# Kernel tuning notes

Measured on AMD Instinct MI355X. Metric: run time of the kernel, lower is better.

## Reference

```python
import jax, jax.numpy as jnp
import numpy as np

S, D, H, C, A = 2048, 256, 8, 64, 16  # seq_len, node_dim, num_heads, num_channels, num_aux


def setup_inputs() -> dict:
    key = jax.random.key(0)
    ks = jax.random.split(key, 11)
    w = 0.02
    return {
        "nodes": jax.random.normal(ks[0], (S, D), jnp.float32),
        "pos": jax.random.uniform(ks[1], (S, 3), jnp.float32),
        "aux": jax.random.normal(ks[2], (S, A), jnp.float32),
        # eqx.nn.Linear weights are (out_features, in_features); y = W @ x + b
        "W_nodes_kq": jax.random.normal(ks[3], (2 * H * C, D), jnp.float32) * w,
        "b_nodes_kq": jax.random.normal(ks[4], (2 * H * C,), jnp.float32) * w,
        "W_pos_kq": jax.random.normal(ks[5], (2 * H * C, 6), jnp.float32) * w,
        "b_pos_kq": jax.random.normal(ks[6], (2 * H * C,), jnp.float32) * w,
        "W_aux_kq": jax.random.normal(ks[7], (2 * H * C, A), jnp.float32) * w,  # no bias
        "W_val": jax.random.normal(ks[8], (D * H * 3, D), jnp.float32) * w,
        "b_val": jax.random.normal(ks[9], (D * H * 3,), jnp.float32) * w,
        "num_heads": H,
    }


def reference(nodes, pos, aux, W_nodes_kq, b_nodes_kq, W_pos_kq, b_pos_kq,
              W_aux_kq, W_val, b_val, num_heads):
    seq_len = nodes.shape[0]
    # circular positional featurization: [S, 6]
    pos_f = jnp.concatenate([jnp.cos(2 * jnp.pi * pos), jnp.sin(2 * jnp.pi * pos)], axis=-1)
    # values: [S, 3*H, D]
    val = (nodes @ W_val.T + b_val).reshape(seq_len, 3 * num_heads, -1)
    # k/q projections, each reshaped [S, H, 2C] then split into k, q of [S, H, C]
    nodes_k, nodes_q = jnp.split((nodes @ W_nodes_kq.T + b_nodes_kq).reshape(seq_len, num_heads, -1), 2, -1)
    pos_k, pos_q = jnp.split((pos_f @ W_pos_kq.T + b_pos_kq).reshape(seq_len, num_heads, -1), 2, -1)
    aux_k, aux_q = jnp.split((aux @ W_aux_kq.T).reshape(seq_len, num_heads, -1), 2, -1)
    # concat along the HEAD axis -> [S, 3H, C]
    k = jnp.concatenate([nodes_k, pos_k, aux_k], axis=-2)
    q = jnp.concatenate([nodes_q, pos_q, aux_q], axis=-2)
    # all-pairs logits [S, S, 3H]; softmax over the SECOND (query, j) index
    logits = jnp.einsum('ihc,jhc->ijh', k, q)
    att = jax.nn.softmax(logits, axis=-2)
    # weighted sum over j and heads -> [S, D]
    out = jnp.einsum('ijh,jhd->id', att, val)
    return out
```

## Files before the change

kernel.cpp:

```cpp
#include <hip/hip_runtime.h>
#include <math.h>

#define SLEN 2048
#define ND 256
#define NH 24
#define HC 64
#define TWO_PI 6.283185307179586f
#define NT 64

typedef __attribute__((ext_vector_type(8))) short short8;
typedef __attribute__((ext_vector_type(16))) float f32x16;
typedef __attribute__((ext_vector_type(2))) unsigned int uint2e;

static __device__ __forceinline__ unsigned short f2bf(float f) {
    union { float f; unsigned int u; } v; v.f = f;
    unsigned int u = v.u;
    return (unsigned short)((u + 0x7FFFu + ((u >> 16) & 1u)) >> 16);
}
static __device__ __forceinline__ unsigned int pack2(float a, float b) {
    return (unsigned int)f2bf(a) | ((unsigned int)f2bf(b) << 16);
}
static __device__ __forceinline__ unsigned int cvtpk(float lo, float hi) {
    unsigned int r;
    asm("v_cvt_pk_bf16_f32 %0, %1, %2" : "=v"(r) : "v"(lo), "v"(hi));
    return r;
}
static __device__ __forceinline__ void gload_lds16(const void* g, void* l) {
    __builtin_amdgcn_global_load_lds(
        (const __attribute__((address_space(1))) void*)(g),
        (__attribute__((address_space(3))) void*)(l), 16, 0, 0);
}

__global__ __launch_bounds__(256) void zero_partial_kernel(float4* __restrict__ p) {
    p[(size_t)blockIdx.x * 256 + threadIdx.x] = make_float4(0.f, 0.f, 0.f, 0.f);
}

__global__ __launch_bounds__(256) void f32_to_bf16_kernel(
    const float4* __restrict__ in, uint2* __restrict__ out) {
    const size_t id = (size_t)blockIdx.x * 256 + threadIdx.x;
    float4 v = in[id];
    uint2 u; u.x = pack2(v.x, v.y); u.y = pack2(v.z, v.w);
    out[id] = u;
}

__global__ __launch_bounds__(256) void posf_kernel(
    const float* __restrict__ pos, float* __restrict__ pos_f) {
    const int s = blockIdx.x * 256 + threadIdx.x;
    if (s < SLEN) {
        #pragma unroll
        for (int c = 0; c < 3; ++c) {
            float v = pos[s * 3 + c] * TWO_PI;
            pos_f[s * 8 + c] = cosf(v);
            pos_f[s * 8 + 3 + c] = sinf(v);
        }
        pos_f[s * 8 + 6] = 0.f; pos_f[s * 8 + 7] = 0.f;
    }
}

__global__ __launch_bounds__(256) void gemm_kernel(
    const unsigned short* __restrict__ wv_bf, const unsigned short* __restrict__ wn_bf,
    const unsigned short* __restrict__ nodes_bf, const float* __restrict__ bv,
    unsigned short* __restrict__ vt, float* __restrict__ kqtmp)
{
    __shared__ __align__(16) char lds[131072];
    const int tid = threadIdx.x;
    const int w = tid >> 6, lane = tid & 63;
    const int l31 = lane & 31, lh = lane >> 5;
    const int bid = blockIdx.x;
    const bool isval = bid < 768;
    int o0, s0;
    const unsigned short *Aptr, *Bptr;
    if (isval) {
        const int wg = ((bid & 7) * 96) + (bid >> 3);
        o0 = (wg >> 4) * 128; s0 = (wg & 15) * 128;
        Aptr = wv_bf + (size_t)o0 * 256; Bptr = nodes_bf + (size_t)s0 * 256;
    } else {
        const int b = bid - 768;
        o0 = (b >> 4) * 128; s0 = (b & 15) * 128;
        Aptr = nodes_bf + (size_t)s0 * 256; Bptr = wn_bf + (size_t)o0 * 256;
    }

    {
        const int rbase = w * 32;
        const int roff = lane >> 5;
        const int slot = l31 * 16;
        #pragma unroll
        for (int i = 0; i < 16; ++i) {
            const int row = rbase + i * 2 + roff;
            const int colb = slot ^ ((row & 31) << 4);
            gload_lds16(Aptr + (((size_t)row) << 8) + (colb >> 1),
                        lds + (rbase + i * 2) * 512);
        }
        #pragma unroll
        for (int i = 0; i < 16; ++i) {
            const int row = rbase + i * 2 + roff;
            const int colb = slot ^ ((row & 31) << 4);
            gload_lds16(Bptr + (((size_t)row) << 8) + (colb >> 1),
                        lds + 65536 + (rbase + i * 2) * 512);
        }
    }
    __syncthreads();

    const int wm = w >> 1, wn = w & 1;
    f32x16 acc[2][2];
    #pragma unroll
    for (int mf = 0; mf < 2; ++mf)
        #pragma unroll
        for (int nf = 0; nf < 2; ++nf)
            #pragma unroll
            for (int r = 0; r < 16; ++r) acc[mf][nf][r] = 0.f;

    const char* Abase = lds;
    const char* Bbase = lds + 65536;
    #pragma unroll
    for (int kk = 0; kk < 16; ++kk) {
        short8 af[2], bq[2];
        #pragma unroll
        for (int mf = 0; mf < 2; ++mf) {
            const int row = wm * 64 + mf * 32 + l31;
            af[mf] = *(const short8*)(Abase + row * 512 +
                     ((kk * 32 + lh * 16) ^ ((row & 31) << 4)));
        }
        #pragma unroll
        for (int nf = 0; nf < 2; ++nf) {
            const int row = wn * 64 + nf * 32 + l31;
            bq[nf] = *(const short8*)(Bbase + row * 512 +
                     ((kk * 32 + lh * 16) ^ ((row & 31) << 4)));
        }
        #pragma unroll
        for (int mf = 0; mf < 2; ++mf)
            #pragma unroll
            for (int nf = 0; nf < 2; ++nf)
                acc[mf][nf] = __builtin_amdgcn_mfma_f32_32x32x16_bf16(
                    af[mf], bq[nf], acc[mf][nf], 0, 0, 0);
    }

    if (isval) {
        #pragma unroll
        for (int mf = 0; mf < 2; ++mf) {
            #pragma unroll
            for (int r = 0; r < 16; ++r) {
                const int o = o0 + wm * 64 + mf * 32 + (r & 3) + 8 * (r >> 2) + 4 * lh;
                const float b = bv[o];
                #pragma unroll
                for (int nf = 0; nf < 2; ++nf) {
                    const int s = s0 + wn * 64 + nf * 32 + l31;
                    vt[(size_t)o * SLEN + s] = f2bf(acc[mf][nf][r] + b);
                }
            }
        }
    } else {
        #pragma unroll
        for (int mf = 0; mf < 2; ++mf) {
            #pragma unroll
            for (int r = 0; r < 16; ++r) {
                const int srow = s0 + wm * 64 + mf * 32 + (r & 3) + 8 * (r >> 2) + 4 * lh;
                #pragma unroll
                for (int nf = 0; nf < 2; ++nf) {
                    const int o = o0 + wn * 64 + nf * 32 + l31;
                    kqtmp[(size_t)srow * 1024 + o] = acc[mf][nf][r];
                }
            }
        }
    }
}

__global__ __launch_bounds__(256) void kq_epi_kernel(
    const float* __restrict__ kqtmp, const float* __restrict__ pos_f,
    const float* __restrict__ aux, const float* __restrict__ bn,
    const float* __restrict__ bp, const float* __restrict__ Wp,
    const float* __restrict__ Wa,
    unsigned short* __restrict__ kbf, unsigned short* __restrict__ qbf)
{
    const int tid = threadIdx.x;
    const int s = blockIdx.x >> 2;
    const int o = (blockIdx.x & 3) * 256 + tid;

    const float vn = kqtmp[(size_t)s * 1024 + o] + bn[o];
    float vp = bp[o];
    #pragma unroll
    for (int d = 0; d < 6; ++d) vp += pos_f[s * 8 + d] * Wp[o * 6 + d];
    float va = 0.f;
    #pragma unroll
    for (int d = 0; d < 16; ++d) va += aux[s * 16 + d] * Wa[o * 16 + d];

    const int h8 = o >> 7, rem = o & 127, isq = rem >> 6, c = rem & 63;
    unsigned short* dst = isq ? qbf : kbf;
    dst[((size_t)h8 * SLEN + s) * HC + c]        = f2bf(vn);
    dst[((size_t)(8 + h8) * SLEN + s) * HC + c]  = f2bf(vp);
    dst[((size_t)(16 + h8) * SLEN + s) * HC + c] = f2bf(va);
}

__global__ __launch_bounds__(256, 3) void attn_kernel(
    const unsigned short* __restrict__ kbf, const unsigned short* __restrict__ qbf,
    const unsigned short* __restrict__ vt, float* __restrict__ partial)
{
    __shared__ __align__(16) char smem[40960];

    const int tid = threadIdx.x;
    const int w = tid >> 6, lane = tid & 63;
    const int l31 = lane & 31, lh = lane >> 5;
    const int wi = w >> 1, wd = w & 1;
    const int wg = (blockIdx.x & 7) * 96 + (blockIdx.x >> 3);
    const int h = wg >> 5, it = wg & 31;
    const int i0 = it * 64;

    const unsigned short* kh = kbf + (size_t)h * SLEN * HC;
    const unsigned short* qh = qbf + (size_t)h * SLEN * HC;
    const unsigned short* vh = vt + (size_t)h * ND * SLEN;

    short8 kf[4];
    {
        const unsigned short* kp = kh + (size_t)(i0 + wi * 32 + l31) * HC + lh * 8;
        #pragma unroll
        for (int ks = 0; ks < 4; ++ks) kf[ks] = *(const short8*)(kp + ks * 16);
    }

    f32x16 acc[4];
    #pragma unroll
    for (int nf = 0; nf < 4; ++nf)
        #pragma unroll
        for (int r = 0; r < 16; ++r) acc[nf][r] = 0.f;
    float m_run = -1e30f, l_run = 0.f;

    auto stage = [&](int bufo, int jt) {
        const int j0n = jt * 32;
        #pragma unroll
        for (int i = 0; i < 5; ++i) {
            const int c = i * 4 + w;
            const int lrow = (lane >> 3);
            const int cu = (((lane & 7) << 4) ^ (lrow << 4));
            if (c < 4) {
                const int row = c * 8 + lrow;
                gload_lds16(qh + (size_t)(j0n + row) * HC + (cu >> 1),
                            smem + bufo + c * 1024);
            } else {
                const int row = (c - 4) * 8 + lrow;
                const int d = row * 2 + (cu >> 6);
                const int j = (cu & 63) >> 1;
                gload_lds16(vh + (size_t)d * SLEN + j0n + j,
                            smem + bufo + 4096 + (c - 4) * 1024);
            }
        }
    };

    auto softpack = [&](f32x16& S, uint4& p0, uint4& p1) {
        float tmax = S[0];
        #pragma unroll
        for (int r = 1; r < 16; ++r) tmax = fmaxf(tmax, S[r]);
        tmax = fmaxf(tmax, __shfl_xor(tmax, 32));
        if (!__all(tmax - m_run <= 8.0f)) {
            const float mnew = fmaxf(m_run, tmax);
            const float sc = __expf(m_run - mnew);
            l_run *= sc; m_run = mnew;
            #pragma unroll
            for (int r = 0; r < 16; ++r) {
                const float scv = __shfl(sc, (r & 3) + 8 * (r >> 2) + 4 * lh);
                #pragma unroll
                for (int nf = 0; nf < 4; ++nf) acc[nf][r] *= scv;
            }
        }
        float psum = 0.f;
        #pragma unroll
        for (int r = 0; r < 16; ++r) {
            S[r] = __expf(S[r] - m_run);
            psum += S[r];
        }
        psum += __shfl_xor(psum, 32);
        l_run += psum;
        uint2e r1 = __builtin_amdgcn_permlane32_swap(cvtpk(S[0], S[1]), cvtpk(S[4], S[5]), false, false);
        uint2e r2 = __builtin_amdgcn_permlane32_swap(cvtpk(S[2], S[3]), cvtpk(S[6], S[7]), false, false);
        uint2e r3 = __builtin_amdgcn_permlane32_swap(cvtpk(S[8], S[9]), cvtpk(S[12], S[13]), false, false);
        uint2e r4 = __builtin_amdgcn_permlane32_swap(cvtpk(S[10], S[11]), cvtpk(S[14], S[15]), false, false);
        p0 = make_uint4(r1[0], r2[0], r1[1], r2[1]);
        p1 = make_uint4(r3[0], r4[0], r3[1], r4[1]);
    };

    stage(0, 0);
    __syncthreads();

    for (int jt = 0; jt < NT; ++jt) {
        const int bo = (jt & 1) * 20480;
        if (jt + 1 < NT) stage(20480 - bo, jt + 1);
        const char* qb = smem + bo;
        const char* vb = smem + bo + 4096;

        f32x16 S;
        #pragma unroll
        for (int r = 0; r < 16; ++r) S[r] = 0.f;
        const int qsw = (l31 & 7) << 4;
        __builtin_amdgcn_s_setprio(1);
        #pragma unroll
        for (int ks = 0; ks < 4; ++ks) {
            short8 a = *(const short8*)(qb + l31 * 128 + ((ks * 32 + lh * 16) ^ qsw));
            S = __builtin_amdgcn_mfma_f32_32x32x16_bf16(a, kf[ks], S, 0, 0, 0);
        }
        __builtin_amdgcn_s_setprio(0);

        uint4 p0, p1;
        softpack(S, p0, p1);

        __builtin_amdgcn_s_setprio(1);
        #pragma unroll
        for (int ksl = 0; ksl < 2; ++ksl) {
            const short8 pa = *(const short8*)(ksl ? &p1 : &p0);
            #pragma unroll
            for (int nf = 0; nf < 4; ++nf) {
                const int d = wd * 128 + nf * 32 + l31;
                const int row = d >> 1;
                const int colb = (((d & 1) << 6) + ksl * 32 + lh * 16) ^ ((row & 7) << 4);
                short8 vfrag = *(const short8*)(vb + row * 128 + colb);
                acc[nf] = __builtin_amdgcn_mfma_f32_32x32x16_bf16(pa, vfrag, acc[nf], 0, 0, 0);
            }
        }
        __builtin_amdgcn_s_setprio(0);
        __syncthreads();
    }

    float* pb = partial + (size_t)(h / 3) * (SLEN * ND);
    const float invm = 1.0f / l_run;
    float lv[16];
    #pragma unroll
    for (int r = 0; r < 16; ++r)
        lv[r] = __shfl(invm, (r & 3) + 8 * (r >> 2) + 4 * lh);
    #pragma unroll
    for (int nf = 0; nf < 4; ++nf) {
        const int d = wd * 128 + nf * 32 + l31;
        #pragma unroll
        for (int r = 0; r < 16; ++r) {
            const int i = i0 + wi * 32 + (r & 3) + 8 * (r >> 2) + 4 * lh;
            atomicAdd(pb + (size_t)i * ND + d, acc[nf][r] * lv[r]);
        }
    }
}

__global__ __launch_bounds__(256) void reduce_kernel(
    const float4* __restrict__ partial, float4* __restrict__ out)
{
    const size_t id = (size_t)blockIdx.x * 256 + threadIdx.x;
    float4 s = make_float4(0.f, 0.f, 0.f, 0.f);
    #pragma unroll
    for (int g = 0; g < 8; ++g) {
        float4 v = partial[g * (SLEN * ND / 4) + id];
        s.x += v.x; s.y += v.y; s.z += v.z; s.w += v.w;
    }
    out[id] = s;
}

extern "C" void kernel_launch(void* const* d_in, const int* in_sizes, int n_in,
                              void* d_out, int out_size, void* d_ws, size_t ws_size,
                              hipStream_t stream) {
    const float* nodes = (const float*)d_in[0];
    const float* pos   = (const float*)d_in[1];
    const float* aux   = (const float*)d_in[2];
    const float* Wn    = (const float*)d_in[3];
    const float* bn    = (const float*)d_in[4];
    const float* Wp    = (const float*)d_in[5];
    const float* bp    = (const float*)d_in[6];
    const float* Wa    = (const float*)d_in[7];
    const float* Wv    = (const float*)d_in[8];
    const float* bv    = (const float*)d_in[9];
    float* out = (float*)d_out;

    const size_t KQ   = (size_t)SLEN * NH * HC;
    const size_t VT   = (size_t)NH * ND * SLEN;
    const size_t WVBF = (size_t)6144 * ND;
    const size_t WNBF = (size_t)1024 * ND;
    const size_t NDBF = (size_t)SLEN * ND;
    const size_t POSF = (size_t)SLEN * 8;
    const size_t KQT  = (size_t)SLEN * 1024;
    const size_t PART = (size_t)8 * SLEN * ND;
    const size_t need = (2 * KQ + VT + WVBF + WNBF + NDBF) * 2 + (POSF + KQT + PART) * 4;

    if (ws_size < need) return;

    unsigned short* kbf = (unsigned short*)d_ws;
    unsigned short* qbf = kbf + KQ;
    unsigned short* vt  = qbf + KQ;
    unsigned short* wv_bf = vt + VT;
    unsigned short* wn_bf = wv_bf + WVBF;
    unsigned short* nodes_bf = wn_bf + WNBF;
    float* pos_f   = (float*)(nodes_bf + NDBF);
    float* kqtmp   = pos_f + POSF;
    float* partial = kqtmp + KQT;

    zero_partial_kernel<<<PART / 1024, 256, 0, stream>>>((float4*)partial);
    f32_to_bf16_kernel<<<1536, 256, 0, stream>>>((const float4*)Wv, (uint2*)wv_bf);
    f32_to_bf16_kernel<<<256, 256, 0, stream>>>((const float4*)Wn, (uint2*)wn_bf);
    f32_to_bf16_kernel<<<512, 256, 0, stream>>>((const float4*)nodes, (uint2*)nodes_bf);
    posf_kernel<<<8, 256, 0, stream>>>(pos, pos_f);
    gemm_kernel<<<896, 256, 0, stream>>>(wv_bf, wn_bf, nodes_bf, bv, vt, kqtmp);
    kq_epi_kernel<<<8192, 256, 0, stream>>>(kqtmp, pos_f, aux, bn, bp, Wp, Wa, kbf, qbf);
    attn_kernel<<<768, 256, 0, stream>>>(kbf, qbf, vt, partial);
    reduce_kernel<<<512, 256, 0, stream>>>((const float4*)partial, (float4*)out);
}
```

Before: 173.5 us.

## Fuse k/q epilogue into GEMM and split softmax from PV across attention waves

```diff
diff --git a/kernel.cpp b/kernel.cpp
--- a/kernel.cpp
+++ b/kernel.cpp
@@ -6,6 +6,7 @@
 #define NH 24
 #define HC 64
 #define TWO_PI 6.283185307179586f
+#define LOG2E 1.4426950408889634f
 #define NT 64
 
 typedef __attribute__((ext_vector_type(8))) short short8;
@@ -29,10 +30,6 @@
     __builtin_amdgcn_global_load_lds(
         (const __attribute__((address_space(1))) void*)(g),
         (__attribute__((address_space(3))) void*)(l), 16, 0, 0);
-}
-
-__global__ __launch_bounds__(256) void zero_partial_kernel(float4* __restrict__ p) {
-    p[(size_t)blockIdx.x * 256 + threadIdx.x] = make_float4(0.f, 0.f, 0.f, 0.f);
 }
 
 __global__ __launch_bounds__(256) void f32_to_bf16_kernel(
@@ -60,7 +57,11 @@
 __global__ __launch_bounds__(256) void gemm_kernel(
     const unsigned short* __restrict__ wv_bf, const unsigned short* __restrict__ wn_bf,
     const unsigned short* __restrict__ nodes_bf, const float* __restrict__ bv,
-    unsigned short* __restrict__ vt, float* __restrict__ kqtmp)
+    unsigned short* __restrict__ vt,
+    const float* __restrict__ pos_f, const float* __restrict__ aux,
+    const float* __restrict__ bn, const float* __restrict__ bp,
+    const float* __restrict__ Wp, const float* __restrict__ Wa,
+    unsigned short* __restrict__ kbf, unsigned short* __restrict__ qbf)
 {
     __shared__ __align__(16) char lds[131072];
     const int tid = threadIdx.x;
@@ -150,52 +151,57 @@
             }
         }
     } else {
-        #pragma unroll
-        for (int mf = 0; mf < 2; ++mf) {
-            #pragma unroll
-            for (int r = 0; r < 16; ++r) {
-                const int srow = s0 + wm * 64 + mf * 32 + (r & 3) + 8 * (r >> 2) + 4 * lh;
+        __syncthreads();
+        float* pa_lds = (float*)lds;
+        for (int i = tid; i < 128 * 6; i += 256) {
+            const int srow = i / 6, q4 = i % 6;
+            float4 v;
+            if (q4 < 2) v = *(const float4*)(pos_f + (size_t)(s0 + srow) * 8 + q4 * 4);
+            else        v = *(const float4*)(aux + (size_t)(s0 + srow) * 16 + (q4 - 2) * 4);
+            *(float4*)(pa_lds + srow * 24 + q4 * 4) = v;
+        }
+        __syncthreads();
+        #pragma unroll
+        for (int nf = 0; nf < 2; ++nf) {
+            const int o = o0 + wn * 64 + nf * 32 + l31;
+            float wp[6], wa[16];
+            #pragma unroll
+            for (int d = 0; d < 6; ++d) wp[d] = Wp[(size_t)o * 6 + d];
+            #pragma unroll
+            for (int d = 0; d < 16; ++d) wa[d] = Wa[(size_t)o * 16 + d];
+            const float bno = bn[o], bpo = bp[o];
+            const int h8 = o >> 7, rem = o & 127, isq = rem >> 6, c = rem & 63;
+            unsigned short* dst = isq ? qbf : kbf;
+            const float ksc = isq ? 1.0f : LOG2E;
+            #pragma unroll
+            for (int mf = 0; mf < 2; ++mf) {
                 #pragma unroll
-                for (int nf = 0; nf < 2; ++nf) {
-                    const int o = o0 + wn * 64 + nf * 32 + l31;
-                    kqtmp[(size_t)srow * 1024 + o] = acc[mf][nf][r];
+                for (int r = 0; r < 16; ++r) {
+                    const int sl = wm * 64 + mf * 32 + (r & 3) + 8 * (r >> 2) + 4 * lh;
+                    const int s = s0 + sl;
+                    const float* pr = pa_lds + sl * 24;
+                    const float vn = acc[mf][nf][r] + bno;
+                    float vp = bpo;
+                    #pragma unroll
+                    for (int d = 0; d < 6; ++d) vp += pr[d] * wp[d];
+                    float va = 0.f;
+                    #pragma unroll
+                    for (int d = 0; d < 16; ++d) va += pr[8 + d] * wa[d];
+                    dst[((size_t)h8 * SLEN + s) * HC + c]        = f2bf(vn * ksc);
+                    dst[((size_t)(8 + h8) * SLEN + s) * HC + c]  = f2bf(vp * ksc);
+                    dst[((size_t)(16 + h8) * SLEN + s) * HC + c] = f2bf(va * ksc);
                 }
             }
         }
     }
-}
-
-__global__ __launch_bounds__(256) void kq_epi_kernel(
-    const float* __restrict__ kqtmp, const float* __restrict__ pos_f,
-    const float* __restrict__ aux, const float* __restrict__ bn,
-    const float* __restrict__ bp, const float* __restrict__ Wp,
-    const float* __restrict__ Wa,
-    unsigned short* __restrict__ kbf, unsigned short* __restrict__ qbf)
-{
-    const int tid = threadIdx.x;
-    const int s = blockIdx.x >> 2;
-    const int o = (blockIdx.x & 3) * 256 + tid;
-
-    const float vn = kqtmp[(size_t)s * 1024 + o] + bn[o];
-    float vp = bp[o];
-    #pragma unroll
-    for (int d = 0; d < 6; ++d) vp += pos_f[s * 8 + d] * Wp[o * 6 + d];
-    float va = 0.f;
-    #pragma unroll
-    for (int d = 0; d < 16; ++d) va += aux[s * 16 + d] * Wa[o * 16 + d];
-
-    const int h8 = o >> 7, rem = o & 127, isq = rem >> 6, c = rem & 63;
-    unsigned short* dst = isq ? qbf : kbf;
-    dst[((size_t)h8 * SLEN + s) * HC + c]        = f2bf(vn);
-    dst[((size_t)(8 + h8) * SLEN + s) * HC + c]  = f2bf(vp);
-    dst[((size_t)(16 + h8) * SLEN + s) * HC + c] = f2bf(va);
 }
 
 __global__ __launch_bounds__(256, 3) void attn_kernel(
     const unsigned short* __restrict__ kbf, const unsigned short* __restrict__ qbf,
     const unsigned short* __restrict__ vt, float* __restrict__ partial)
 {
-    __shared__ __align__(16) char smem[40960];
+    __shared__ __align__(16) char smem[45312];
+    const int BUF = 20480, VOFF = 4096, POFF = 40960, SCOFF = 45056;
 
     const int tid = threadIdx.x;
     const int w = tid >> 6, lane = tid & 63;
@@ -223,82 +229,114 @@
         for (int r = 0; r < 16; ++r) acc[nf][r] = 0.f;
     float m_run = -1e30f, l_run = 0.f;
 
+    auto stage_chunk = [&](int bufo, int j0n, int c) {
+        if (c < 4) {
+            const int row = c * 8 + (lane >> 3);
+            const int cb = ((lane & 7) << 4) ^ ((row & 7) << 4);
+            gload_lds16(qh + (size_t)(j0n + row) * HC + (cb >> 1),
+                        smem + bufo + c * 1024);
+        } else {
+            const int cc = c - 4;
+            const int d = cc * 16 + (lane >> 2);
+            const int jb = ((lane & 3) << 4) ^ (((d >> 1) & 3) << 4);
+            gload_lds16(vh + (size_t)d * SLEN + j0n + (jb >> 1),
+                        smem + bufo + VOFF + cc * 1024);
+        }
+    };
     auto stage = [&](int bufo, int jt) {
         const int j0n = jt * 32;
-        #pragma unroll
-        for (int i = 0; i < 5; ++i) {
-            const int c = i * 4 + w;
-            const int lrow = (lane >> 3);
-            const int cu = (((lane & 7) << 4) ^ (lrow << 4));
-            if (c < 4) {
-                const int row = c * 8 + lrow;
-                gload_lds16(qh + (size_t)(j0n + row) * HC + (cu >> 1),
-                            smem + bufo + c * 1024);
-            } else {
-                const int row = (c - 4) * 8 + lrow;
-                const int d = row * 2 + (cu >> 6);
-                const int j = (cu & 63) >> 1;
-                gload_lds16(vh + (size_t)d * SLEN + j0n + j,
-                            smem + bufo + 4096 + (c - 4) * 1024);
-            }
-        }
-    };
-
-    auto softpack = [&](f32x16& S, uint4& p0, uint4& p1) {
-        float tmax = S[0];
-        #pragma unroll
-        for (int r = 1; r < 16; ++r) tmax = fmaxf(tmax, S[r]);
-        tmax = fmaxf(tmax, __shfl_xor(tmax, 32));
-        if (!__all(tmax - m_run <= 8.0f)) {
-            const float mnew = fmaxf(m_run, tmax);
-            const float sc = __expf(m_run - mnew);
-            l_run *= sc; m_run = mnew;
-            #pragma unroll
-            for (int r = 0; r < 16; ++r) {
-                const float scv = __shfl(sc, (r & 3) + 8 * (r >> 2) + 4 * lh);
-                #pragma unroll
-                for (int nf = 0; nf < 4; ++nf) acc[nf][r] *= scv;
-            }
-        }
-        float psum = 0.f;
-        #pragma unroll
-        for (int r = 0; r < 16; ++r) {
-            S[r] = __expf(S[r] - m_run);
-            psum += S[r];
-        }
-        psum += __shfl_xor(psum, 32);
-        l_run += psum;
-        uint2e r1 = __builtin_amdgcn_permlane32_swap(cvtpk(S[0], S[1]), cvtpk(S[4], S[5]), false, false);
-        uint2e r2 = __builtin_amdgcn_permlane32_swap(cvtpk(S[2], S[3]), cvtpk(S[6], S[7]), false, false);
-        uint2e r3 = __builtin_amdgcn_permlane32_swap(cvtpk(S[8], S[9]), cvtpk(S[12], S[13]), false, false);
-        uint2e r4 = __builtin_amdgcn_permlane32_swap(cvtpk(S[10], S[11]), cvtpk(S[14], S[15]), false, false);
-        p0 = make_uint4(r1[0], r2[0], r1[1], r2[1]);
-        p1 = make_uint4(r3[0], r4[0], r3[1], r4[1]);
+        if (wd == 0) {
+            const int st = (w == 0) ? 0 : 10;
+            #pragma unroll
+            for (int i = 0; i < 3; ++i) stage_chunk(bufo, j0n, st + i);
+        } else {
+            const int st = (w == 1) ? 3 : 13;
+            #pragma unroll
+            for (int i = 0; i < 7; ++i) stage_chunk(bufo, j0n, st + i);
+        }
     };
 
     stage(0, 0);
     __syncthreads();
 
     for (int jt = 0; jt < NT; ++jt) {
-        const int bo = (jt & 1) * 20480;
-        if (jt + 1 < NT) stage(20480 - bo, jt + 1);
+        const int bo = (jt & 1) * BUF;
+        if (jt + 1 < NT) stage(BUF - bo, jt + 1);
         const char* qb = smem + bo;
-        const char* vb = smem + bo + 4096;
-
-        f32x16 S;
-        #pragma unroll
-        for (int r = 0; r < 16; ++r) S[r] = 0.f;
-        const int qsw = (l31 & 7) << 4;
-        __builtin_amdgcn_s_setprio(1);
-        #pragma unroll
-        for (int ks = 0; ks < 4; ++ks) {
-            short8 a = *(const short8*)(qb + l31 * 128 + ((ks * 32 + lh * 16) ^ qsw));
-            S = __builtin_amdgcn_mfma_f32_32x32x16_bf16(a, kf[ks], S, 0, 0, 0);
-        }
-        __builtin_amdgcn_s_setprio(0);
+        const char* vb = smem + bo + VOFF;
 
         uint4 p0, p1;
-        softpack(S, p0, p1);
+        if (wd == 0) {
+            f32x16 S;
+            #pragma unroll
+            for (int r = 0; r < 16; ++r) S[r] = 0.f;
+            const int qsw = (l31 & 7) << 4;
+            __builtin_amdgcn_s_setprio(1);
+            #pragma unroll
+            for (int ks = 0; ks < 4; ++ks) {
+                short8 a = *(const short8*)(qb + l31 * 128 + ((ks * 32 + lh * 16) ^ qsw));
+                S = __builtin_amdgcn_mfma_f32_32x32x16_bf16(a, kf[ks], S, 0, 0, 0);
+            }
+            __builtin_amdgcn_s_setprio(0);
+
+            float t0 = fmaxf(fmaxf(S[0], S[1]), S[2]);
+            float t1 = fmaxf(fmaxf(S[3], S[4]), S[5]);
+            float t2 = fmaxf(fmaxf(S[6], S[7]), S[8]);
+            float t3 = fmaxf(fmaxf(S[9], S[10]), S[11]);
+            float t4 = fmaxf(fmaxf(S[12], S[13]), S[14]);
+            float tmax = fmaxf(fmaxf(fmaxf(t0, t1), fmaxf(t2, t3)), fmaxf(t4, S[15]));
+            tmax = fmaxf(tmax, __shfl_xor(tmax, 32));
+
+            float scw = 1.0f;
+            if (!__all(tmax - m_run <= 8.0f)) {
+                const float mnew = fmaxf(m_run, tmax);
+                scw = exp2f(m_run - mnew);
+                l_run *= scw; m_run = mnew;
+                #pragma unroll
+                for (int r = 0; r < 16; ++r) {
+                    const float scv = __shfl(scw, (r & 3) + 8 * (r >> 2) + 4 * lh);
+                    #pragma unroll
+                    for (int nf = 0; nf < 4; ++nf) acc[nf][r] *= scv;
+                }
+            }
+            if (lane < 32) *(float*)(smem + SCOFF + wi * 128 + l31 * 4) = scw;
+
+            float psum = 0.f;
+            #pragma unroll
+            for (int r = 0; r < 16; ++r) {
+                S[r] = exp2f(S[r] - m_run);
+                psum += S[r];
+            }
+            psum += __shfl_xor(psum, 32);
+            l_run += psum;
+
+            uint2e r1 = __builtin_amdgcn_permlane32_swap(cvtpk(S[0], S[1]), cvtpk(S[4], S[5]), false, false);
+            uint2e r2 = __builtin_amdgcn_permlane32_swap(cvtpk(S[2], S[3]), cvtpk(S[6], S[7]), false, false);
+            uint2e r3 = __builtin_amdgcn_permlane32_swap(cvtpk(S[8], S[9]), cvtpk(S[12], S[13]), false, false);
+            uint2e r4 = __builtin_amdgcn_permlane32_swap(cvtpk(S[10], S[11]), cvtpk(S[14], S[15]), false, false);
+            p0 = make_uint4(r1[0], r2[0], r1[1], r2[1]);
+            p1 = make_uint4(r3[0], r4[0], r3[1], r4[1]);
+            *(uint4*)(smem + POFF + wi * 2048 + lane * 16) = p0;
+            *(uint4*)(smem + POFF + wi * 2048 + 1024 + lane * 16) = p1;
+        }
+
+        asm volatile("s_waitcnt lgkmcnt(0)" ::: "memory");
+        __builtin_amdgcn_s_barrier();
+        asm volatile("" ::: "memory");
+
+        if (wd == 1) {
+            p0 = *(const uint4*)(smem + POFF + wi * 2048 + lane * 16);
+            p1 = *(const uint4*)(smem + POFF + wi * 2048 + 1024 + lane * 16);
+            const float scr = *(const float*)(smem + SCOFF + wi * 128 + l31 * 4);
+            if (!__all(scr == 1.0f)) {
+                #pragma unroll
+                for (int r = 0; r < 16; ++r) {
+                    const float scv = __shfl(scr, (r & 3) + 8 * (r >> 2) + 4 * lh);
+                    #pragma unroll
+                    for (int nf = 0; nf < 4; ++nf) acc[nf][r] *= scv;
+                }
+            }
+        }
 
         __builtin_amdgcn_s_setprio(1);
         #pragma unroll
@@ -307,9 +345,8 @@
             #pragma unroll
             for (int nf = 0; nf < 4; ++nf) {
                 const int d = wd * 128 + nf * 32 + l31;
-                const int row = d >> 1;
-                const int colb = (((d & 1) << 6) + ksl * 32 + lh * 16) ^ ((row & 7) << 4);
-                short8 vfrag = *(const short8*)(vb + row * 128 + colb);
+                const int slot = (ksl * 32 + lh * 16) ^ (((d >> 1) & 3) << 4);
+                short8 vfrag = *(const short8*)(vb + d * 64 + slot);
                 acc[nf] = __builtin_amdgcn_mfma_f32_32x32x16_bf16(pa, vfrag, acc[nf], 0, 0, 0);
             }
         }
@@ -317,12 +354,15 @@
         __syncthreads();
     }
 
+    if (wd == 0 && lane < 32)
+        *(float*)(smem + SCOFF + wi * 128 + l31 * 4) = 1.0f / l_run;
+    __syncthreads();
+    const float invl = *(const float*)(smem + SCOFF + wi * 128 + l31 * 4);
+    float lv[16];
+    #pragma unroll
+    for (int r = 0; r < 16; ++r)
+        lv[r] = __shfl(invl, (r & 3) + 8 * (r >> 2) + 4 * lh);
     float* pb = partial + (size_t)(h / 3) * (SLEN * ND);
-    const float invm = 1.0f / l_run;
-    float lv[16];
-    #pragma unroll
-    for (int r = 0; r < 16; ++r)
-        lv[r] = __shfl(invm, (r & 3) + 8 * (r >> 2) + 4 * lh);
     #pragma unroll
     for (int nf = 0; nf < 4; ++nf) {
         const int d = wd * 128 + nf * 32 + l31;
@@ -368,9 +408,8 @@
     const size_t WNBF = (size_t)1024 * ND;
     const size_t NDBF = (size_t)SLEN * ND;
     const size_t POSF = (size_t)SLEN * 8;
-    const size_t KQT  = (size_t)SLEN * 1024;
     const size_t PART = (size_t)8 * SLEN * ND;
-    const size_t need = (2 * KQ + VT + WVBF + WNBF + NDBF) * 2 + (POSF + KQT + PART) * 4;
+    const size_t need = (2 * KQ + VT + WVBF + WNBF + NDBF) * 2 + (POSF + PART) * 4;
 
     if (ws_size < need) return;
 
@@ -381,16 +420,15 @@
     unsigned short* wn_bf = wv_bf + WVBF;
     unsigned short* nodes_bf = wn_bf + WNBF;
     float* pos_f   = (float*)(nodes_bf + NDBF);
-    float* kqtmp   = pos_f + POSF;
-    float* partial = kqtmp + KQT;
-
-    zero_partial_kernel<<<PART / 1024, 256, 0, stream>>>((float4*)partial);
+    float* partial = pos_f + POSF;
+
+    hipMemsetAsync(partial, 0, PART * sizeof(float), stream);
     f32_to_bf16_kernel<<<1536, 256, 0, stream>>>((const float4*)Wv, (uint2*)wv_bf);
     f32_to_bf16_kernel<<<256, 256, 0, stream>>>((const float4*)Wn, (uint2*)wn_bf);
     f32_to_bf16_kernel<<<512, 256, 0, stream>>>((const float4*)nodes, (uint2*)nodes_bf);
     posf_kernel<<<8, 256, 0, stream>>>(pos, pos_f);
-    gemm_kernel<<<896, 256, 0, stream>>>(wv_bf, wn_bf, nodes_bf, bv, vt, kqtmp);
-    kq_epi_kernel<<<8192, 256, 0, stream>>>(kqtmp, pos_f, aux, bn, bp, Wp, Wa, kbf, qbf);
+    gemm_kernel<<<896, 256, 0, stream>>>(wv_bf, wn_bf, nodes_bf, bv, vt,
+                                         pos_f, aux, bn, bp, Wp, Wa, kbf, qbf);
     attn_kernel<<<768, 256, 0, stream>>>(kbf, qbf, vt, partial);
     reduce_kernel<<<512, 256, 0, stream>>>((const float4*)partial, (float4*)out);
 }
```

New measurement: 305.1 us. 1.76x slower.

## Fuse node k/q bias epilogue into GEMM and switch softmax to exp2

Applied to the files above, without the earlier changes.

```diff
diff --git a/kernel.cpp b/kernel.cpp
--- a/kernel.cpp
+++ b/kernel.cpp
@@ -6,6 +6,7 @@
 #define NH 24
 #define HC 64
 #define TWO_PI 6.283185307179586f
+#define LOG2E 1.4426950408889634f
 #define NT 64
 
 typedef __attribute__((ext_vector_type(8))) short short8;
@@ -25,14 +26,13 @@
     asm("v_cvt_pk_bf16_f32 %0, %1, %2" : "=v"(r) : "v"(lo), "v"(hi));
     return r;
 }
+static __device__ __forceinline__ float exp2fast(float x) {
+    return __builtin_amdgcn_exp2f(x);
+}
 static __device__ __forceinline__ void gload_lds16(const void* g, void* l) {
     __builtin_amdgcn_global_load_lds(
         (const __attribute__((address_space(1))) void*)(g),
         (__attribute__((address_space(3))) void*)(l), 16, 0, 0);
-}
-
-__global__ __launch_bounds__(256) void zero_partial_kernel(float4* __restrict__ p) {
-    p[(size_t)blockIdx.x * 256 + threadIdx.x] = make_float4(0.f, 0.f, 0.f, 0.f);
 }
 
 __global__ __launch_bounds__(256) void f32_to_bf16_kernel(
@@ -60,7 +60,8 @@
 __global__ __launch_bounds__(256) void gemm_kernel(
     const unsigned short* __restrict__ wv_bf, const unsigned short* __restrict__ wn_bf,
     const unsigned short* __restrict__ nodes_bf, const float* __restrict__ bv,
-    unsigned short* __restrict__ vt, float* __restrict__ kqtmp)
+    unsigned short* __restrict__ vt, const float* __restrict__ bn,
+    unsigned short* __restrict__ kbf, unsigned short* __restrict__ qbf)
 {
     __shared__ __align__(16) char lds[131072];
     const int tid = threadIdx.x;
@@ -151,44 +152,47 @@
         }
     } else {
         #pragma unroll
-        for (int mf = 0; mf < 2; ++mf) {
-            #pragma unroll
-            for (int r = 0; r < 16; ++r) {
-                const int srow = s0 + wm * 64 + mf * 32 + (r & 3) + 8 * (r >> 2) + 4 * lh;
+        for (int nf = 0; nf < 2; ++nf) {
+            const int o = o0 + wn * 64 + nf * 32 + l31;
+            const float bno = bn[o];
+            const int h8 = o >> 7, isq = (o >> 6) & 1, c = o & 63;
+            unsigned short* dst = isq ? qbf : kbf;
+            const float ksc = isq ? 1.0f : LOG2E;
+            #pragma unroll
+            for (int mf = 0; mf < 2; ++mf) {
                 #pragma unroll
-                for (int nf = 0; nf < 2; ++nf) {
-                    const int o = o0 + wn * 64 + nf * 32 + l31;
-                    kqtmp[(size_t)srow * 1024 + o] = acc[mf][nf][r];
+                for (int r = 0; r < 16; ++r) {
+                    const int s = s0 + wm * 64 + mf * 32 + (r & 3) + 8 * (r >> 2) + 4 * lh;
+                    dst[((size_t)h8 * SLEN + s) * HC + c] = f2bf((acc[mf][nf][r] + bno) * ksc);
                 }
             }
         }
     }
 }
 
-__global__ __launch_bounds__(256) void kq_epi_kernel(
-    const float* __restrict__ kqtmp, const float* __restrict__ pos_f,
-    const float* __restrict__ aux, const float* __restrict__ bn,
+__global__ __launch_bounds__(256) void pa_kernel(
+    const float* __restrict__ pos_f, const float* __restrict__ aux,
     const float* __restrict__ bp, const float* __restrict__ Wp,
     const float* __restrict__ Wa,
     unsigned short* __restrict__ kbf, unsigned short* __restrict__ qbf)
 {
-    const int tid = threadIdx.x;
-    const int s = blockIdx.x >> 2;
-    const int o = (blockIdx.x & 3) * 256 + tid;
-
-    const float vn = kqtmp[(size_t)s * 1024 + o] + bn[o];
-    float vp = bp[o];
-    #pragma unroll
-    for (int d = 0; d < 6; ++d) vp += pos_f[s * 8 + d] * Wp[o * 6 + d];
-    float va = 0.f;
-    #pragma unroll
-    for (int d = 0; d < 16; ++d) va += aux[s * 16 + d] * Wa[o * 16 + d];
-
-    const int h8 = o >> 7, rem = o & 127, isq = rem >> 6, c = rem & 63;
+    const int s = blockIdx.x >> 3;
+    const int o2 = (blockIdx.x & 7) * 256 + threadIdx.x;
+    const int op = o2 & 1023;
+    const int h8 = op >> 7, isq = (op >> 6) & 1, c = op & 63;
     unsigned short* dst = isq ? qbf : kbf;
-    dst[((size_t)h8 * SLEN + s) * HC + c]        = f2bf(vn);
-    dst[((size_t)(8 + h8) * SLEN + s) * HC + c]  = f2bf(vp);
-    dst[((size_t)(16 + h8) * SLEN + s) * HC + c] = f2bf(va);
+    const float ksc = isq ? 1.0f : LOG2E;
+    if (o2 < 1024) {
+        float v = bp[op];
+        #pragma unroll
+        for (int d = 0; d < 6; ++d) v += pos_f[s * 8 + d] * Wp[op * 6 + d];
+        dst[((size_t)(8 + h8) * SLEN + s) * HC + c] = f2bf(v * ksc);
+    } else {
+        float v = 0.f;
+        #pragma unroll
+        for (int d = 0; d < 16; ++d) v += aux[s * 16 + d] * Wa[op * 16 + d];
+        dst[((size_t)(16 + h8) * SLEN + s) * HC + c] = f2bf(v * ksc);
+    }
 }
 
 __global__ __launch_bounds__(256, 3) void attn_kernel(
@@ -196,6 +200,7 @@
     const unsigned short* __restrict__ vt, float* __restrict__ partial)
 {
     __shared__ __align__(16) char smem[40960];
+    const int BUF = 20480, VOFF = 4096;
 
     const int tid = threadIdx.x;
     const int w = tid >> 6, lane = tid & 63;
@@ -239,7 +244,7 @@
                 const int d = row * 2 + (cu >> 6);
                 const int j = (cu & 63) >> 1;
                 gload_lds16(vh + (size_t)d * SLEN + j0n + j,
-                            smem + bufo + 4096 + (c - 4) * 1024);
+                            smem + bufo + VOFF + (c - 4) * 1024);
             }
         }
     };
@@ -251,7 +256,7 @@
         tmax = fmaxf(tmax, __shfl_xor(tmax, 32));
         if (!__all(tmax - m_run <= 8.0f)) {
             const float mnew = fmaxf(m_run, tmax);
-            const float sc = __expf(m_run - mnew);
+            const float sc = exp2fast(m_run - mnew);
             l_run *= sc; m_run = mnew;
             #pragma unroll
             for (int r = 0; r < 16; ++r) {
@@ -263,7 +268,7 @@
         float psum = 0.f;
         #pragma unroll
         for (int r = 0; r < 16; ++r) {
-            S[r] = __expf(S[r] - m_run);
+            S[r] = exp2fast(S[r] - m_run);
             psum += S[r];
         }
         psum += __shfl_xor(psum, 32);
@@ -280,10 +285,10 @@
     __syncthreads();
 
     for (int jt = 0; jt < NT; ++jt) {
-        const int bo = (jt & 1) * 20480;
-        if (jt + 1 < NT) stage(20480 - bo, jt + 1);
+        const int bo = (jt & 1) * BUF;
+        if (jt + 1 < NT) stage(BUF - bo, jt + 1);
         const char* qb = smem + bo;
-        const char* vb = smem + bo + 4096;
+        const char* vb = smem + bo + VOFF;
 
         f32x16 S;
         #pragma unroll
@@ -368,9 +373,8 @@
     const size_t WNBF = (size_t)1024 * ND;
     const size_t NDBF = (size_t)SLEN * ND;
     const size_t POSF = (size_t)SLEN * 8;
-    const size_t KQT  = (size_t)SLEN * 1024;
     const size_t PART = (size_t)8 * SLEN * ND;
-    const size_t need = (2 * KQ + VT + WVBF + WNBF + NDBF) * 2 + (POSF + KQT + PART) * 4;
+    const size_t need = (2 * KQ + VT + WVBF + WNBF + NDBF) * 2 + (POSF + PART) * 4;
 
     if (ws_size < need) return;
 
@@ -381,16 +385,15 @@
     unsigned short* wn_bf = wv_bf + WVBF;
     unsigned short* nodes_bf = wn_bf + WNBF;
     float* pos_f   = (float*)(nodes_bf + NDBF);
-    float* kqtmp   = pos_f + POSF;
-    float* partial = kqtmp + KQT;
-
-    zero_partial_kernel<<<PART / 1024, 256, 0, stream>>>((float4*)partial);
+    float* partial = pos_f + POSF;
+
+    hipMemsetAsync(partial, 0, PART * sizeof(float), stream);
     f32_to_bf16_kernel<<<1536, 256, 0, stream>>>((const float4*)Wv, (uint2*)wv_bf);
     f32_to_bf16_kernel<<<256, 256, 0, stream>>>((const float4*)Wn, (uint2*)wn_bf);
     f32_to_bf16_kernel<<<512, 256, 0, stream>>>((const float4*)nodes, (uint2*)nodes_bf);
     posf_kernel<<<8, 256, 0, stream>>>(pos, pos_f);
-    gemm_kernel<<<896, 256, 0, stream>>>(wv_bf, wn_bf, nodes_bf, bv, vt, kqtmp);
-    kq_epi_kernel<<<8192, 256, 0, stream>>>(kqtmp, pos_f, aux, bn, bp, Wp, Wa, kbf, qbf);
+    gemm_kernel<<<896, 256, 0, stream>>>(wv_bf, wn_bf, nodes_bf, bv, vt, bn, kbf, qbf);
+    pa_kernel<<<16384, 256, 0, stream>>>(pos_f, aux, bp, Wp, Wa, kbf, qbf);
     attn_kernel<<<768, 256, 0, stream>>>(kbf, qbf, vt, partial);
     reduce_kernel<<<512, 256, 0, stream>>>((const float4*)partial, (float4*)out);
 }
```

After: 180.3 us. +3.9%, slower.
